# Performance work log

Measured on AMD Instinct MI355X. Metric: run time of the kernel, lower is better.

## Reference

```python
import math
import jax, jax.numpy as jnp
import numpy as np

HEADS = 8


def setup_inputs() -> dict:
    key = jax.random.key(0)
    k1, k2, k3 = jax.random.split(key, 3)
    b, n, a, dim = 1, 256, 256, 512
    init_scale = 0.02
    x = jax.random.normal(k1, (b, n, a, dim), dtype=jnp.float32)
    w_qkv = jax.random.normal(k2, (dim, 3 * dim), dtype=jnp.float32) * init_scale
    b_qkv = jnp.zeros((3 * dim,), dtype=jnp.float32)
    w_proj = jax.random.normal(k3, (dim, dim), dtype=jnp.float32) * init_scale
    b_proj = jnp.zeros((dim,), dtype=jnp.float32)
    return {"x": x, "w_qkv": w_qkv, "b_qkv": b_qkv, "w_proj": w_proj, "b_proj": b_proj}


def reference(x, w_qkv, b_qkv, w_proj, b_proj):
    b, n, a, dim = x.shape
    dh = dim // HEADS
    scale = 1.0 / math.sqrt(math.sqrt(dh))
    qkv = jnp.einsum('bnad,de->bnae', x, w_qkv) + b_qkv  # [b,n,a,3*dim]
    qkv = qkv.reshape(b, n, a, HEADS, 3 * dh)
    q, k, v = jnp.split(qkv, 3, axis=-1)  # each [b,n,a,h,dh]
    # scores over the 'a' axis, independent per (b, n, head)
    sim = jnp.einsum('bnihd,bnjhd->bnhij', q * scale, k * scale)
    attn = jax.nn.softmax(sim, axis=-1)
    out = jnp.einsum('bnhij,bnjhd->bnihd', attn, v).reshape(b, n, a, dim)
    return jnp.einsum('bnad,de->bnae', out, w_proj) + b_proj
```

## Files before the change

kernel.cpp:

```cpp
#include <hip/hip_runtime.h>

typedef unsigned short u16;
typedef unsigned int u32;
typedef __bf16 bf16x8 __attribute__((ext_vector_type(8)));
typedef float f32x4 __attribute__((ext_vector_type(4)));

__device__ __forceinline__ u16 f2b(float f) {
  u32 u = __builtin_bit_cast(u32, f);
  u32 r = (u + 0x7fffu + ((u >> 16) & 1u)) >> 16;
  return (u16)r;
}
__device__ __forceinline__ bf16x8 ld_frag(const u16* p) {
  uint4 v = *(const uint4*)p;
  return __builtin_bit_cast(bf16x8, v);
}
__device__ __forceinline__ void async_lds16(const u16* g, u16* lds) {
  __builtin_amdgcn_global_load_lds(
      (const __attribute__((address_space(1))) void*)g,
      (__attribute__((address_space(3))) void*)lds, 16, 0, 0);
}
__device__ __forceinline__ void wait_lds() { __builtin_amdgcn_s_waitcnt(0xc07f); }

__global__ __launch_bounds__(256) void convert_f32_bf16(const float* __restrict__ in,
                                                        u16* __restrict__ out) {
  long i = ((long)blockIdx.x * 256 + threadIdx.x) * 8;
  float4 a = *(const float4*)(in + i);
  float4 b = *(const float4*)(in + i + 4);
  union { uint4 v; u16 e[8]; } u;
  u.e[0] = f2b(a.x); u.e[1] = f2b(a.y); u.e[2] = f2b(a.z); u.e[3] = f2b(a.w);
  u.e[4] = f2b(b.x); u.e[5] = f2b(b.y); u.e[6] = f2b(b.z); u.e[7] = f2b(b.w);
  *(uint4*)(out + i) = u.v;
}

__global__ __launch_bounds__(256) void transpose_w(const float* __restrict__ W,
                                                   u16* __restrict__ Wt,
                                                   int K, int N) {
  __shared__ alignas(16) u16 T[64][80];
  const int n0 = blockIdx.x * 64, k0 = blockIdx.y * 64;
  const int t = threadIdx.x;
  {
    int kk = t >> 3, c = t & 7;
#pragma unroll
    for (int rr = 0; rr < 2; ++rr) {
      int kr = kk + rr * 32;
      const float* src = W + (long)(k0 + kr) * N + n0 + c * 8;
      float4 a = *(const float4*)src;
      float4 b = *(const float4*)(src + 4);
      u16* dst = &T[kr][c * 8];
      dst[0] = f2b(a.x); dst[1] = f2b(a.y); dst[2] = f2b(a.z); dst[3] = f2b(a.w);
      dst[4] = f2b(b.x); dst[5] = f2b(b.y); dst[6] = f2b(b.z); dst[7] = f2b(b.w);
    }
  }
  __syncthreads();
  {
    int nn = t >> 3, kc = t & 7;
#pragma unroll
    for (int rr = 0; rr < 2; ++rr) {
      int nr = nn + rr * 32;
      union { uint4 v; u16 e[8]; } u;
#pragma unroll
      for (int i = 0; i < 8; ++i) u.e[i] = T[kc * 8 + i][nr];
      *(uint4*)(Wt + (long)(n0 + nr) * K + k0 + kc * 8) = u.v;
    }
  }
}

template <bool OUT_F32>
__global__ __launch_bounds__(512, 2) void gemm_pipe(const u16* __restrict__ A,
                                                    const u16* __restrict__ Bt,
                                                    const float* __restrict__ bias,
                                                    void* __restrict__ Cv,
                                                    int M, int N, int K) {
  __shared__ alignas(16) u16 lds[3 * 24576];
  const int tid = threadIdx.x;
  const int lane = tid & 63, wave = tid >> 6;
  const int quad = lane >> 4, ln = lane & 15;
  const int wm = wave >> 1, wn = wave & 1;

  const int nwg = gridDim.x;
  const int bid = blockIdx.x;
  const int wg = (bid & 7) * (nwg >> 3) + (bid >> 3);
  const int ntn = N >> 7;
  const int tn = wg % ntn, tm = wg / ntn;
  const long m0 = (long)tm * 256;
  const long n0 = (long)tn * 128;

  const int rbase = wave * 8 + (lane >> 3);
  const int swzch = ((lane & 7) ^ ((lane >> 3) & 7)) * 8;
  const u16* gA[4];
  const u16* gB[2];
#pragma unroll
  for (int u = 0; u < 4; ++u) gA[u] = A + (long)(m0 + u * 64 + rbase) * K + swzch;
#pragma unroll
  for (int u = 0; u < 2; ++u) gB[u] = Bt + (long)(n0 + u * 64 + rbase) * K + swzch;

  auto stageA3 = [&](int t) {
    long kst = (long)t * 64;
    u16* sl = &lds[(t % 3) * 24576 + wave * 512];
    async_lds16(gA[0] + kst, sl);
    async_lds16(gA[1] + kst, sl + 4096);
    async_lds16(gA[2] + kst, sl + 8192);
  };
  auto stageRest = [&](int t) {
    long kst = (long)t * 64;
    u16* sl = &lds[(t % 3) * 24576 + wave * 512];
    async_lds16(gA[3] + kst, sl + 12288);
    async_lds16(gB[0] + kst, sl + 16384);
    async_lds16(gB[1] + kst, sl + 16384 + 4096);
  };

  f32x4 zero = {0.f, 0.f, 0.f, 0.f};
  f32x4 acc[4][4];
#pragma unroll
  for (int i = 0; i < 4; ++i)
#pragma unroll
    for (int j = 0; j < 4; ++j) acc[i][j] = zero;

  const int KT = K >> 6;

  stageA3(0); stageRest(0);
  stageA3(1); stageRest(1);
  __builtin_amdgcn_s_waitcnt(0x0f76);
  __builtin_amdgcn_s_barrier();

  for (int t = 0; t < KT; ++t) {
    const u16* sl = &lds[(t % 3) * 24576];
    bf16x8 bfr[4][2], af[2][2];
#pragma unroll
    for (int nt = 0; nt < 4; ++nt)
#pragma unroll
      for (int ks = 0; ks < 2; ++ks) {
        int row = wn * 64 + nt * 16 + ln;
        bfr[nt][ks] = ld_frag(&sl[16384 + row * 64 + (((ks * 4 + quad) ^ (row & 7)) * 8)]);
      }
#pragma unroll
    for (int mt = 0; mt < 2; ++mt)
#pragma unroll
      for (int ks = 0; ks < 2; ++ks) {
        int row = wm * 64 + mt * 16 + ln;
        af[mt][ks] = ld_frag(&sl[row * 64 + (((ks * 4 + quad) ^ (row & 7)) * 8)]);
      }
    if (t + 2 < KT) stageA3(t + 2);
    __builtin_amdgcn_s_barrier();
    __builtin_amdgcn_s_setprio(1);
#pragma unroll
    for (int mt = 0; mt < 2; ++mt)
#pragma unroll
      for (int nt = 0; nt < 4; ++nt)
#pragma unroll
        for (int ks = 0; ks < 2; ++ks)
          acc[mt][nt] = __builtin_amdgcn_mfma_f32_16x16x32_bf16(af[mt][ks], bfr[nt][ks], acc[mt][nt], 0, 0, 0);
    __builtin_amdgcn_s_setprio(0);
    __builtin_amdgcn_s_barrier();
#pragma unroll
    for (int mt = 0; mt < 2; ++mt)
#pragma unroll
      for (int ks = 0; ks < 2; ++ks) {
        int row = wm * 64 + (mt + 2) * 16 + ln;
        af[mt][ks] = ld_frag(&sl[row * 64 + (((ks * 4 + quad) ^ (row & 7)) * 8)]);
      }
    if (t + 2 < KT) stageRest(t + 2);
    __builtin_amdgcn_s_barrier();
    __builtin_amdgcn_s_setprio(1);
#pragma unroll
    for (int mt = 0; mt < 2; ++mt)
#pragma unroll
      for (int nt = 0; nt < 4; ++nt)
#pragma unroll
        for (int ks = 0; ks < 2; ++ks)
          acc[mt + 2][nt] = __builtin_amdgcn_mfma_f32_16x16x32_bf16(af[mt][ks], bfr[nt][ks], acc[mt + 2][nt], 0, 0, 0);
    __builtin_amdgcn_s_setprio(0);
    if (t + 1 < KT) {
      if (t + 2 < KT) __builtin_amdgcn_s_waitcnt(0x0f76);
      else            __builtin_amdgcn_s_waitcnt(0x0f70);
    }
    __builtin_amdgcn_s_barrier();
  }

  __syncthreads();

  if (OUT_F32) {
#pragma unroll
    for (int nt = 0; nt < 4; ++nt) {
      long coln = n0 + wn * 64 + nt * 16 + ln;
      float bv = bias[coln];
#pragma unroll
      for (int mt = 0; mt < 4; ++mt) {
        long rowb = m0 + wm * 64 + mt * 16 + quad * 4;
#pragma unroll
        for (int r = 0; r < 4; ++r)
          ((float*)Cv)[(rowb + r) * N + coln] = acc[mt][nt][r] + bv;
      }
    }
  } else {
    u16* patch = &lds[wave * 2176];
    float bv[4];
#pragma unroll
    for (int nt = 0; nt < 4; ++nt) bv[nt] = bias[n0 + wn * 64 + nt * 16 + ln];
#pragma unroll
    for (int mt = 0; mt < 4; ++mt) {
#pragma unroll
      for (int nt = 0; nt < 4; ++nt)
#pragma unroll
        for (int r = 0; r < 4; ++r)
          patch[(quad * 4 + r) * 136 + nt * 16 + ln] = f2b(acc[mt][nt][r] + bv[nt]);
      wait_lds();
#pragma unroll
      for (int it = 0; it < 2; ++it) {
        int cid = it * 64 + lane;
        int row = cid >> 3, ch = cid & 7;
        uint4 v = *(const uint4*)&patch[row * 136 + ch * 8];
        *(uint4*)&((u16*)Cv)[(m0 + wm * 64 + mt * 16 + row) * (long)N + n0 + wn * 64 + ch * 8] = v;
      }
      wait_lds();
    }
  }
}

__global__ __launch_bounds__(256, 2) void attn_fused(const u16* __restrict__ qkv,
                                                     u16* __restrict__ out) {
  __shared__ alignas(16) u16 Ks[256 * 64];
  __shared__ alignas(16) u16 Vt[64 * 256];
  const int h = blockIdx.x;
  const long n = blockIdx.y;
  const int tid = threadIdx.x;
  const int lane = tid & 63, wave = tid >> 6;
  const int quad = lane >> 4, ln = lane & 15;
  const u16* base = qkv + (n * 256) * 1536 + h * 192;

  auto stageK = [&]() {
    int c = tid & 7, jb = tid >> 3;
#pragma unroll
    for (int rr = 0; rr < 8; ++rr) {
      int j = jb + rr * 32;
      uint4 v = *(const uint4*)(base + (long)j * 1536 + 64 + c * 8);
      *(uint4*)&Ks[j * 64 + ((c ^ (j & 7)) * 8)] = v;
    }
  };
  stageK();
  {
    int p = tid & 7, jb = tid >> 3;
#pragma unroll
    for (int rr = 0; rr < 8; ++rr) {
      int j = jb + rr * 32;
      union { uint4 v; u16 e[8]; } u;
      u.v = *(const uint4*)(base + (long)j * 1536 + 128 + p * 8);
      int cj = j >> 3, jl = j & 7;
#pragma unroll
      for (int i = 0; i < 8; ++i) {
        int d = p * 8 + i;
        int key = (p ^ i) & 7;
        Vt[d * 256 + ((cj ^ key) * 8) + jl] = u.e[i];
      }
    }
  }
  __syncthreads();

  u16* Pw = &Ks[wave * 2176];
  f32x4 zero = {0.f, 0.f, 0.f, 0.f};

  for (int s = 0; s < 2; ++s) {
    const int row0 = wave * 64 + s * 32;
    bf16x8 qa[2][2];
#pragma unroll
    for (int mt = 0; mt < 2; ++mt)
#pragma unroll
      for (int kc = 0; kc < 2; ++kc)
        qa[mt][kc] = ld_frag(base + (long)(row0 + mt * 16 + ln) * 1536 + kc * 32 + quad * 8);

    f32x4 sacc[2][16];
#pragma unroll
    for (int mt = 0; mt < 2; ++mt)
#pragma unroll
      for (int jt = 0; jt < 16; ++jt) sacc[mt][jt] = zero;

#pragma unroll
    for (int jt = 0; jt < 16; ++jt) {
#pragma unroll
      for (int kc = 0; kc < 2; ++kc) {
        bf16x8 kb = ld_frag(&Ks[(jt * 16 + ln) * 64 + (((kc * 4 + quad) ^ (ln & 7)) * 8)]);
        sacc[0][jt] = __builtin_amdgcn_mfma_f32_16x16x32_bf16(qa[0][kc], kb, sacc[0][jt], 0, 0, 0);
        sacc[1][jt] = __builtin_amdgcn_mfma_f32_16x16x32_bf16(qa[1][kc], kb, sacc[1][jt], 0, 0, 0);
      }
    }
    __syncthreads();

#pragma unroll
    for (int mt = 0; mt < 2; ++mt) {
      float linv[4];
#pragma unroll
      for (int r = 0; r < 4; ++r) {
        float mx = -3.0e38f;
#pragma unroll
        for (int jt = 0; jt < 16; ++jt) mx = fmaxf(mx, sacc[mt][jt][r]);
        mx = fmaxf(mx, __shfl_xor(mx, 1));
        mx = fmaxf(mx, __shfl_xor(mx, 2));
        mx = fmaxf(mx, __shfl_xor(mx, 4));
        mx = fmaxf(mx, __shfl_xor(mx, 8));
        float l = 0.f;
#pragma unroll
        for (int jt = 0; jt < 16; ++jt) {
          float p = __expf((sacc[mt][jt][r] - mx) * 0.125f);
          sacc[mt][jt][r] = p;
          l += p;
        }
        l += __shfl_xor(l, 1);
        l += __shfl_xor(l, 2);
        l += __shfl_xor(l, 4);
        l += __shfl_xor(l, 8);
        linv[r] = 1.0f / l;
      }

      f32x4 oacc[4];
#pragma unroll
      for (int dt = 0; dt < 4; ++dt) oacc[dt] = zero;
#pragma unroll
      for (int jh = 0; jh < 2; ++jh) {
#pragma unroll
        for (int jl = 0; jl < 8; ++jl) {
          int jt = jh * 8 + jl;
#pragma unroll
          for (int r = 0; r < 4; ++r)
            Pw[(quad * 4 + r) * 136 + jl * 16 + ln] = f2b(sacc[mt][jt][r]);
        }
        wait_lds();
#pragma unroll
        for (int jcl = 0; jcl < 4; ++jcl) {
          bf16x8 pa = ld_frag(&Pw[ln * 136 + jcl * 32 + quad * 8]);
          int cjb = (jh * 4 + jcl) * 4 + quad;
#pragma unroll
          for (int dt = 0; dt < 4; ++dt) {
            int d = dt * 16 + ln;
            int key = ((d >> 3) ^ d) & 7;
            bf16x8 vb = ld_frag(&Vt[d * 256 + ((cjb ^ key) * 8)]);
            oacc[dt] = __builtin_amdgcn_mfma_f32_16x16x32_bf16(pa, vb, oacc[dt], 0, 0, 0);
          }
        }
      }
#pragma unroll
      for (int dt = 0; dt < 4; ++dt)
#pragma unroll
        for (int r = 0; r < 4; ++r)
          Pw[(quad * 4 + r) * 136 + dt * 16 + ln] = f2b(oacc[dt][r] * linv[r]);
      wait_lds();
#pragma unroll
      for (int it = 0; it < 2; ++it) {
        int cid = it * 64 + lane;
        int row = cid >> 3, ch = cid & 7;
        uint4 v = *(const uint4*)&Pw[row * 136 + ch * 8];
        *(uint4*)&out[(n * 256 + row0 + mt * 16 + row) * 512 + h * 64 + ch * 8] = v;
      }
    }
    __syncthreads();
    if (s == 0) {
      stageK();
      __syncthreads();
    }
  }
}

extern "C" void kernel_launch(void* const* d_in, const int* in_sizes, int n_in,
                              void* d_out, int out_size, void* d_ws, size_t ws_size,
                              hipStream_t stream) {
  const float* x      = (const float*)d_in[0];
  const float* w_qkv  = (const float*)d_in[1];
  const float* b_qkv  = (const float*)d_in[2];
  const float* w_proj = (const float*)d_in[3];
  const float* b_proj = (const float*)d_in[4];
  float* out = (float*)d_out;

  char* ws = (char*)d_ws;
  u16* xb   = (u16*)ws;
  u16* qkv  = (u16*)(ws + 67108864L);
  u16* attn = (u16*)(ws + 67108864L + 201326592L);
  u16* Wt1  = (u16*)(ws + 67108864L + 201326592L + 67108864L);
  u16* Wt2  = Wt1 + 1536 * 512;

  convert_f32_bf16<<<16384, 256, 0, stream>>>(x, xb);
  transpose_w<<<dim3(24, 8), 256, 0, stream>>>(w_qkv, Wt1, 512, 1536);
  transpose_w<<<dim3(8, 8), 256, 0, stream>>>(w_proj, Wt2, 512, 512);
  gemm_pipe<false><<<dim3(12 * 256), 512, 0, stream>>>(xb, Wt1, b_qkv, qkv, 65536, 1536, 512);
  attn_fused<<<dim3(8, 256), 256, 0, stream>>>(qkv, attn);
  gemm_pipe<true><<<dim3(4 * 256), 512, 0, stream>>>(attn, Wt2, b_proj, out, 65536, 512, 512);
}
```

Baseline: 570.2 us.

## Restructure GEMM to 4-wave blocks with 128x64 warp tiles and register-prefetched fragments

The GEMM kernel moves from 8 waves to 4 waves per 256x128 tile. Each wave now computes a 128x64 sub-tile with 32 accumulators. The K step drops from 64 to 32, which halves the LDS stage size, and a new XOR swizzle matches the shorter rows. The main loop prefetches the next step's A and B fragments into registers while the MFMAs for the upper half run, so there are fewer barriers per step. The aim is more MFMA work per LDS read and less synchronisation, at the cost of much higher register pressure and a longer dependence chain per wave.

```diff
diff --git a/kernel.cpp b/kernel.cpp
--- a/kernel.cpp
+++ b/kernel.cpp
@@ -66,12 +66,12 @@
 }
 
 template <bool OUT_F32>
-__global__ __launch_bounds__(512, 2) void gemm_pipe(const u16* __restrict__ A,
+__global__ __launch_bounds__(256, 2) void gemm_pipe(const u16* __restrict__ A,
                                                     const u16* __restrict__ Bt,
                                                     const float* __restrict__ bias,
                                                     void* __restrict__ Cv,
                                                     int M, int N, int K) {
-  __shared__ alignas(16) u16 lds[3 * 24576];
+  __shared__ alignas(16) u16 lds[3 * 12288];
   const int tid = threadIdx.x;
   const int lane = tid & 63, wave = tid >> 6;
   const int quad = lane >> 4, ln = lane & 15;
@@ -85,96 +85,98 @@
   const long m0 = (long)tm * 256;
   const long n0 = (long)tn * 128;
 
-  const int rbase = wave * 8 + (lane >> 3);
-  const int swzch = ((lane & 7) ^ ((lane >> 3) & 7)) * 8;
+  const int srow = lane >> 2;
+  const int swz = ((lane & 3) ^ (srow & 3)) * 8;
   const u16* gA[4];
   const u16* gB[2];
 #pragma unroll
-  for (int u = 0; u < 4; ++u) gA[u] = A + (long)(m0 + u * 64 + rbase) * K + swzch;
-#pragma unroll
-  for (int u = 0; u < 2; ++u) gB[u] = Bt + (long)(n0 + u * 64 + rbase) * K + swzch;
-
-  auto stageA3 = [&](int t) {
-    long kst = (long)t * 64;
-    u16* sl = &lds[(t % 3) * 24576 + wave * 512];
-    async_lds16(gA[0] + kst, sl);
-    async_lds16(gA[1] + kst, sl + 4096);
-    async_lds16(gA[2] + kst, sl + 8192);
-  };
-  auto stageRest = [&](int t) {
-    long kst = (long)t * 64;
-    u16* sl = &lds[(t % 3) * 24576 + wave * 512];
-    async_lds16(gA[3] + kst, sl + 12288);
-    async_lds16(gB[0] + kst, sl + 16384);
-    async_lds16(gB[1] + kst, sl + 16384 + 4096);
+  for (int u = 0; u < 4; ++u) gA[u] = A + (long)(m0 + u * 64 + wave * 16 + srow) * K + swz;
+#pragma unroll
+  for (int v = 0; v < 2; ++v) gB[v] = Bt + (long)(n0 + v * 64 + wave * 16 + srow) * K + swz;
+
+  const int KT = K >> 5;
+
+  auto stageP1 = [&](int t) {
+    if (t >= KT) return;
+    u16* s = &lds[(t % 3) * 12288 + wave * 512];
+    long ko = (long)t * 32;
+    async_lds16(gA[0] + ko, s);
+    async_lds16(gA[1] + ko, s + 2048);
+    async_lds16(gA[2] + ko, s + 4096);
+  };
+  auto stageP2 = [&](int t) {
+    if (t >= KT) return;
+    u16* s = &lds[(t % 3) * 12288 + wave * 512];
+    long ko = (long)t * 32;
+    async_lds16(gA[3] + ko, s + 6144);
+    async_lds16(gB[0] + ko, s + 8192);
+    async_lds16(gB[1] + ko, s + 8192 + 2048);
+  };
+
+  const int cswz = (quad ^ (ln & 3)) * 8;
+  auto ldA = [&](int t, int mt) {
+    int row = wm * 128 + mt * 16 + ln;
+    return ld_frag(&lds[(t % 3) * 12288 + row * 32 + cswz]);
+  };
+  auto ldB = [&](int t, int nt) {
+    int row = wn * 64 + nt * 16 + ln;
+    return ld_frag(&lds[(t % 3) * 12288 + 8192 + row * 32 + cswz]);
   };
 
   f32x4 zero = {0.f, 0.f, 0.f, 0.f};
-  f32x4 acc[4][4];
-#pragma unroll
-  for (int i = 0; i < 4; ++i)
+  f32x4 acc[8][4];
+#pragma unroll
+  for (int i = 0; i < 8; ++i)
 #pragma unroll
     for (int j = 0; j < 4; ++j) acc[i][j] = zero;
 
-  const int KT = K >> 6;
-
-  stageA3(0); stageRest(0);
-  stageA3(1); stageRest(1);
+  stageP1(0); stageP2(0);
+  stageP1(1); stageP2(1);
   __builtin_amdgcn_s_waitcnt(0x0f76);
   __builtin_amdgcn_s_barrier();
 
+  bf16x8 bf[4], alo[4], ahi[4];
+#pragma unroll
+  for (int nt = 0; nt < 4; ++nt) bf[nt] = ldB(0, nt);
+#pragma unroll
+  for (int mt = 0; mt < 4; ++mt) alo[mt] = ldA(0, mt);
+
   for (int t = 0; t < KT; ++t) {
-    const u16* sl = &lds[(t % 3) * 24576];
-    bf16x8 bfr[4][2], af[2][2];
-#pragma unroll
-    for (int nt = 0; nt < 4; ++nt)
-#pragma unroll
-      for (int ks = 0; ks < 2; ++ks) {
-        int row = wn * 64 + nt * 16 + ln;
-        bfr[nt][ks] = ld_frag(&sl[16384 + row * 64 + (((ks * 4 + quad) ^ (row & 7)) * 8)]);
-      }
-#pragma unroll
-    for (int mt = 0; mt < 2; ++mt)
-#pragma unroll
-      for (int ks = 0; ks < 2; ++ks) {
-        int row = wm * 64 + mt * 16 + ln;
-        af[mt][ks] = ld_frag(&sl[row * 64 + (((ks * 4 + quad) ^ (row & 7)) * 8)]);
-      }
-    if (t + 2 < KT) stageA3(t + 2);
-    __builtin_amdgcn_s_barrier();
-    __builtin_amdgcn_s_setprio(1);
-#pragma unroll
-    for (int mt = 0; mt < 2; ++mt)
+#pragma unroll
+    for (int mt = 0; mt < 4; ++mt) ahi[mt] = ldA(t, mt + 4);
+    stageP1(t + 2);
+#pragma unroll
+    for (int mt = 0; mt < 4; ++mt)
 #pragma unroll
       for (int nt = 0; nt < 4; ++nt)
-#pragma unroll
-        for (int ks = 0; ks < 2; ++ks)
-          acc[mt][nt] = __builtin_amdgcn_mfma_f32_16x16x32_bf16(af[mt][ks], bfr[nt][ks], acc[mt][nt], 0, 0, 0);
-    __builtin_amdgcn_s_setprio(0);
-    __builtin_amdgcn_s_barrier();
-#pragma unroll
-    for (int mt = 0; mt < 2; ++mt)
-#pragma unroll
-      for (int ks = 0; ks < 2; ++ks) {
-        int row = wm * 64 + (mt + 2) * 16 + ln;
-        af[mt][ks] = ld_frag(&sl[row * 64 + (((ks * 4 + quad) ^ (row & 7)) * 8)]);
-      }
-    if (t + 2 < KT) stageRest(t + 2);
-    __builtin_amdgcn_s_barrier();
-    __builtin_amdgcn_s_setprio(1);
-#pragma unroll
-    for (int mt = 0; mt < 2; ++mt)
-#pragma unroll
-      for (int nt = 0; nt < 4; ++nt)
-#pragma unroll
-        for (int ks = 0; ks < 2; ++ks)
-          acc[mt + 2][nt] = __builtin_amdgcn_mfma_f32_16x16x32_bf16(af[mt][ks], bfr[nt][ks], acc[mt + 2][nt], 0, 0, 0);
-    __builtin_amdgcn_s_setprio(0);
+        acc[mt][nt] = __builtin_amdgcn_mfma_f32_16x16x32_bf16(alo[mt], bf[nt], acc[mt][nt], 0, 0, 0);
     if (t + 1 < KT) {
-      if (t + 2 < KT) __builtin_amdgcn_s_waitcnt(0x0f76);
+      if (t + 2 < KT) __builtin_amdgcn_s_waitcnt(0x0f73);
       else            __builtin_amdgcn_s_waitcnt(0x0f70);
-    }
-    __builtin_amdgcn_s_barrier();
+      wait_lds();
+      __builtin_amdgcn_s_barrier();
+      bf16x8 nbf[4], nalo[4];
+#pragma unroll
+      for (int nt = 0; nt < 4; ++nt) nbf[nt] = ldB(t + 1, nt);
+#pragma unroll
+      for (int mt = 0; mt < 4; ++mt) nalo[mt] = ldA(t + 1, mt);
+      stageP2(t + 2);
+#pragma unroll
+      for (int mt = 0; mt < 4; ++mt)
+#pragma unroll
+        for (int nt = 0; nt < 4; ++nt)
+          acc[mt + 4][nt] = __builtin_amdgcn_mfma_f32_16x16x32_bf16(ahi[mt], bf[nt], acc[mt + 4][nt], 0, 0, 0);
+#pragma unroll
+      for (int nt = 0; nt < 4; ++nt) bf[nt] = nbf[nt];
+#pragma unroll
+      for (int mt = 0; mt < 4; ++mt) alo[mt] = nalo[mt];
+    } else {
+#pragma unroll
+      for (int mt = 0; mt < 4; ++mt)
+#pragma unroll
+        for (int nt = 0; nt < 4; ++nt)
+          acc[mt + 4][nt] = __builtin_amdgcn_mfma_f32_16x16x32_bf16(ahi[mt], bf[nt], acc[mt + 4][nt], 0, 0, 0);
+    }
   }
 
   __syncthreads();
@@ -185,8 +187,8 @@
       long coln = n0 + wn * 64 + nt * 16 + ln;
       float bv = bias[coln];
 #pragma unroll
-      for (int mt = 0; mt < 4; ++mt) {
-        long rowb = m0 + wm * 64 + mt * 16 + quad * 4;
+      for (int mt = 0; mt < 8; ++mt) {
+        long rowb = m0 + wm * 128 + mt * 16 + quad * 4;
 #pragma unroll
         for (int r = 0; r < 4; ++r)
           ((float*)Cv)[(rowb + r) * N + coln] = acc[mt][nt][r] + bv;
@@ -198,7 +200,7 @@
 #pragma unroll
     for (int nt = 0; nt < 4; ++nt) bv[nt] = bias[n0 + wn * 64 + nt * 16 + ln];
 #pragma unroll
-    for (int mt = 0; mt < 4; ++mt) {
+    for (int mt = 0; mt < 8; ++mt) {
 #pragma unroll
       for (int nt = 0; nt < 4; ++nt)
 #pragma unroll
@@ -210,7 +212,7 @@
         int cid = it * 64 + lane;
         int row = cid >> 3, ch = cid & 7;
         uint4 v = *(const uint4*)&patch[row * 136 + ch * 8];
-        *(uint4*)&((u16*)Cv)[(m0 + wm * 64 + mt * 16 + row) * (long)N + n0 + wn * 64 + ch * 8] = v;
+        *(uint4*)&((u16*)Cv)[(m0 + wm * 128 + mt * 16 + row) * (long)N + n0 + wn * 64 + ch * 8] = v;
       }
       wait_lds();
     }
@@ -379,7 +381,7 @@
   convert_f32_bf16<<<16384, 256, 0, stream>>>(x, xb);
   transpose_w<<<dim3(24, 8), 256, 0, stream>>>(w_qkv, Wt1, 512, 1536);
   transpose_w<<<dim3(8, 8), 256, 0, stream>>>(w_proj, Wt2, 512, 512);
-  gemm_pipe<false><<<dim3(12 * 256), 512, 0, stream>>>(xb, Wt1, b_qkv, qkv, 65536, 1536, 512);
+  gemm_pipe<false><<<dim3(12 * 256), 256, 0, stream>>>(xb, Wt1, b_qkv, qkv, 65536, 1536, 512);
   attn_fused<<<dim3(8, 256), 256, 0, stream>>>(qkv, attn);
-  gemm_pipe<true><<<dim3(4 * 256), 512, 0, stream>>>(attn, Wt2, b_proj, out, 65536, 512, 512);
-}
+  gemm_pipe<true><<<dim3(4 * 256), 256, 0, stream>>>(attn, Wt2, b_proj, out, 65536, 512, 512);
+}
```

Result: slower. 593.2 us (+4.0%).
